# Optimization experiments

Hardware: AMD Instinct MI355X
Metric: run time of the kernel (lower is better)

Reference implementation:

```python
import jax, jax.numpy as jnp
import numpy as np

B, N, H, Z, C, IN = 4, 32768, 512, 256, 9, 64
N_TRUNK = 4   # fc_2..fc_5
N_HEADS = 4   # xyz, rgb, scale, opacity (n_layers=1 each)
FACTORS = {'xyz': 1.0, 'rgb': 1.0, 'scale': 1.0, 'opacity': 1.0}


def setup_inputs() -> dict:
    key = jax.random.key(0)
    ks = jax.random.split(key, 20)
    rn = lambda k, s, sc=1.0: jax.random.normal(k, s, jnp.float32) * np.float32(sc)
    wg = 1.0 / np.sqrt(H)       # ModLinear weight_gain / sqrt(in_features)
    sg = 1.0 / np.sqrt(Z)       # style-linear init scale
    inp = {
        'pt_feat': rn(ks[0], (B, N, IN)),
        'onehots': jax.random.uniform(ks[1], (B, N, C), jnp.float32),
        'z': rn(ks[2], (B, Z)),
        'fc1_w': rn(ks[3], (H, IN), 1.0 / np.sqrt(IN)),
        'fc1_b': jnp.zeros((H,), jnp.float32),
        'fcma_w': rn(ks[4], (H, C), 1.0 / np.sqrt(C)),
        # stacked ModLinear params: fc_2..fc_5
        'trunk_weight': rn(ks[5], (N_TRUNK, H, H), wg),
        'trunk_walpha': rn(ks[6], (N_TRUNK, H, Z), sg),
        'trunk_balpha': jnp.ones((N_TRUNK, H), jnp.float32),
        'trunk_wbeta': rn(ks[7], (N_TRUNK, H, Z), sg),
        'trunk_bbeta': jnp.zeros((N_TRUNK, H), jnp.float32),
        # stacked ModLinear params: fc_6_{xyz,rgb,scale,opacity}_0
        'head_weight': rn(ks[8], (N_HEADS, H, H), wg),
        'head_walpha': rn(ks[9], (N_HEADS, H, Z), sg),
        'head_balpha': jnp.ones((N_HEADS, H), jnp.float32),
        'head_wbeta': rn(ks[10], (N_HEADS, H, Z), sg),
        'head_bbeta': jnp.zeros((N_HEADS, H), jnp.float32),
        # output heads
        'out_w_xyz': rn(ks[11], (3, H), 1.0 / np.sqrt(H)),
        'out_b_xyz': jnp.zeros((3,), jnp.float32),
        'out_w_rgb': rn(ks[12], (3, H), 1.0 / np.sqrt(H)),
        'out_b_rgb': jnp.zeros((3,), jnp.float32),
        'out_w_scale': rn(ks[13], (3, H), 1.0 / np.sqrt(H)),
        'out_b_scale': jnp.zeros((3,), jnp.float32),
        'out_w_opacity': rn(ks[14], (1, H), 1.0 / np.sqrt(H)),
        'out_b_opacity': jnp.zeros((1,), jnp.float32),
    }
    return inp


def _act(x):
    # LeakyReLU(0.2)
    return jnp.where(x > 0, x, 0.2 * x)


def _modlin(x, z, W, Wa, ba, Wb, bb):
    """ModLinear with bias=False, mod_bias=True, output_mode=True.
    torch: baddbmm(beta, x, (W*alpha).T) == (x*alpha) @ W.T + beta
    x: [B,N,H], z: [B,Z], W: [H,H], Wa/Wb: [H,Z], ba/bb: [H]."""
    alpha = z @ Wa.T + ba            # [B,H] per-batch input scale
    beta = z @ Wb.T + bb             # [B,H] per-batch output bias
    y = jnp.einsum('bni,oi->bno', x * alpha[:, None, :], W)
    return y + beta[:, None, :]


def reference(pt_feat, onehots, z, fc1_w, fc1_b, fcma_w,
              trunk_weight, trunk_walpha, trunk_balpha, trunk_wbeta, trunk_bbeta,
              head_weight, head_walpha, head_balpha, head_wbeta, head_bbeta,
              out_w_xyz, out_b_xyz, out_w_rgb, out_b_rgb,
              out_w_scale, out_b_scale, out_w_opacity, out_b_opacity):
    f = _act(pt_feat @ fc1_w.T + fc1_b + onehots @ fcma_w.T)  # [B,N,H]
    for i in range(N_TRUNK):
        f = _act(_modlin(f, z, trunk_weight[i], trunk_walpha[i], trunk_balpha[i],
                         trunk_wbeta[i], trunk_bbeta[i]))
    heads = [(out_w_xyz, out_b_xyz), (out_w_rgb, out_b_rgb),
             (out_w_scale, out_b_scale), (out_w_opacity, out_b_opacity)]
    outs = []
    for i, (ow, ob) in enumerate(heads):
        g = _act(_modlin(f, z, head_weight[i], head_walpha[i], head_balpha[i],
                         head_wbeta[i], head_bbeta[i]))
        outs.append(g @ ow.T + ob)
    xyz = (jax.nn.sigmoid(outs[0]) - 0.5) * FACTORS['xyz']
    rgb = outs[1] * FACTORS['rgb']
    scale = jnp.clip(outs[2], 1.0, 1.0)
    opacity = jax.nn.sigmoid(outs[3]) * FACTORS['opacity'] + (1.0 - FACTORS['opacity'])
    # concat dict values in fixed key order (xyz,rgb,scale,opacity) -> [B,N,10]
    return jnp.concatenate([xyz, rgb, scale, opacity], axis=-1)
```

## Files before the change

### kernel.cpp

```cpp
#include <hip/hip_runtime.h>
#include <hip/hip_bf16.h>
#include <cstdint>

#define MTOT 131072
#define MC2  65536
#define MCH  32768
#define HDIM 512

typedef _Float16 f16x8 __attribute__((ext_vector_type(8)));
typedef _Float16 f16x4 __attribute__((ext_vector_type(4)));
typedef unsigned short u16x8 __attribute__((ext_vector_type(8)));
typedef unsigned short u16x4 __attribute__((ext_vector_type(4)));
typedef float    f32x4 __attribute__((ext_vector_type(4)));

__device__ __forceinline__ float bf2f(unsigned short u) {
  return __uint_as_float(((unsigned)u) << 16);
}

__device__ __forceinline__ float ldin(const void* p, long i, int isbf) {
  if (isbf) return bf2f(((const unsigned short*)p)[i]);
  return ((const float*)p)[i];
}

__device__ __forceinline__ void load_lds16(const void* g, void* lds) {
  __builtin_amdgcn_global_load_lds(
      (const __attribute__((address_space(1))) void*)(unsigned long long)(uintptr_t)g,
      (__attribute__((address_space(3))) void*)(unsigned int)(uintptr_t)lds,
      16, 0, 0);
}

__global__ void detect_k(const unsigned* __restrict__ balpha, int* __restrict__ flag) {
  if (threadIdx.x == 0) flag[0] = (balpha[0] == 0x3F803F80u) ? 1 : 0;
}

__global__ __launch_bounds__(256)
void prep_ab(const void* __restrict__ z,
             const void* __restrict__ twa, const void* __restrict__ tba,
             const void* __restrict__ twb, const void* __restrict__ tbb,
             const void* __restrict__ hwa, const void* __restrict__ hba,
             const void* __restrict__ hwb, const void* __restrict__ hbb,
             const int* __restrict__ flag,
             float* __restrict__ alphas, float* __restrict__ betas) {
  const int isbf = flag[0];
  const int bid = blockIdx.x;
  const int og = bid & 7, rest = bid >> 3;
  const int l = rest >> 3, p = (rest >> 2) & 1, b = rest & 3;
  __shared__ float zs[256];
  zs[threadIdx.x] = ldin(z, b * 256 + threadIdx.x, isbf);
  __syncthreads();
  const void *Wsrc, *bsrc;
  long wofs, bofs;
  if (l < 4) {
    Wsrc = (p ? twb : twa); wofs = (long)l * 512 * 256;
    bsrc = (p ? tbb : tba); bofs = l * 512;
  } else {
    const int h = (l == 6) ? 3 : (l - 4);
    Wsrc = (p ? hwb : hwa); wofs = (long)h * 512 * 256;
    bsrc = (p ? hbb : hba); bofs = h * 512;
  }
  const int o = og * 64 + (threadIdx.x >> 2);
  const int kq = threadIdx.x & 3;
  float s = 0.f;
  if (isbf) {
    const unsigned short* wp = (const unsigned short*)Wsrc + wofs + (long)o * 256 + kq * 64;
#pragma unroll
    for (int g = 0; g < 8; g++) {
      u16x8 v = *(const u16x8*)(wp + g * 8);
#pragma unroll
      for (int j = 0; j < 8; j++) s += zs[kq * 64 + g * 8 + j] * bf2f(v[j]);
    }
  } else {
    const float* wp = (const float*)Wsrc + wofs + (long)o * 256 + kq * 64;
#pragma unroll
    for (int g = 0; g < 16; g++) {
      f32x4 v = *(const f32x4*)(wp + g * 4);
#pragma unroll
      for (int j = 0; j < 4; j++) s += zs[kq * 64 + g * 4 + j] * v[j];
    }
  }
  s += __shfl_xor(s, 1, 64);
  s += __shfl_xor(s, 2, 64);
  if (kq == 0) {
    float* dst = (p ? betas : alphas) + (l * 4 + b) * 512;
    dst[o] = s + ldin(bsrc, bofs + o, isbf);
  }
}

__global__ void wmod_k(const void* __restrict__ tw, const void* __restrict__ hw,
                       const int* __restrict__ flag,
                       const float* __restrict__ alphas, _Float16* __restrict__ wmod) {
  const int isbf = flag[0];
  const long t = (long)blockIdx.x * 256 + threadIdx.x;
  const long idx = t * 8;
  const int l   = (int)(idx >> 20);
  const long r0 = idx & ((1 << 20) - 1);
  const int b   = (int)(r0 >> 18);
  const int o   = (int)((r0 >> 9) & 511);
  const int k0  = (int)(r0 & 511);
  const void* wsrc; long ofs;
  if (l < 4) { wsrc = tw; ofs = ((long)l << 18) + (o << 9) + k0; }
  else { const int h = (l == 6) ? 3 : (l - 4); wsrc = hw; ofs = ((long)h << 18) + (o << 9) + k0; }
  const float* al = alphas + (l * 4 + b) * 512 + k0;
  f32x4 a0 = *(const f32x4*)(al);
  f32x4 a1 = *(const f32x4*)(al + 4);
  f16x8 d;
  if (isbf) {
    u16x8 w8 = *(const u16x8*)((const unsigned short*)wsrc + ofs);
#pragma unroll
    for (int j = 0; j < 4; j++) d[j] = (_Float16)(bf2f(w8[j]) * a0[j]);
#pragma unroll
    for (int j = 0; j < 4; j++) d[4 + j] = (_Float16)(bf2f(w8[4 + j]) * a1[j]);
  } else {
    f32x4 w0 = *(const f32x4*)((const float*)wsrc + ofs);
    f32x4 w1 = *(const f32x4*)((const float*)wsrc + ofs + 4);
#pragma unroll
    for (int j = 0; j < 4; j++) d[j] = (_Float16)(w0[j] * a0[j]);
#pragma unroll
    for (int j = 0; j < 4; j++) d[4 + j] = (_Float16)(w1[j] * a1[j]);
  }
  *(f16x8*)(wmod + ((long)(l * 4 + b) << 18) + (o << 9) + k0) = d;
}

__global__ __launch_bounds__(256)
void pack_x(const void* __restrict__ pt, const void* __restrict__ oh,
            long pt_ofs, long oh_ofs, const int* __restrict__ flag,
            _Float16* __restrict__ X) {
  const int isbf = flag[0];
  const int m = blockIdx.x * 8 + (threadIdx.x >> 5);
  const int c5 = threadIdx.x & 31;
  f16x4 d;
  if (c5 < 16) {
    if (isbf) {
      u16x4 v = *(const u16x4*)((const unsigned short*)pt + pt_ofs + (long)m * 64 + c5 * 4);
#pragma unroll
      for (int j = 0; j < 4; j++) d[j] = (_Float16)bf2f(v[j]);
    } else {
      f32x4 v = *(const f32x4*)((const float*)pt + pt_ofs + (long)m * 64 + c5 * 4);
#pragma unroll
      for (int j = 0; j < 4; j++) d[j] = (_Float16)v[j];
    }
  } else {
#pragma unroll
    for (int j = 0; j < 4; j++) {
      const int c = c5 * 4 + j;
      d[j] = (c < 73) ? (_Float16)ldin(oh, oh_ofs + (long)m * 9 + (c - 64), isbf) : (_Float16)0.f;
    }
  }
  *(f16x4*)(X + (long)m * 128 + c5 * 4) = d;
}

__global__ void pack_wc(const void* __restrict__ fc1w, const void* __restrict__ fcmaw,
                        const void* __restrict__ fc1b, const int* __restrict__ flag,
                        _Float16* __restrict__ Wc, float* __restrict__ fb32) {
  const int isbf = flag[0];
  const int o = blockIdx.x, c = threadIdx.x;
  float v = 0.f;
  if (c < 64)      v = ldin(fc1w, o * 64 + c, isbf);
  else if (c < 73) v = ldin(fcmaw, o * 9 + c - 64, isbf);
  Wc[o * 128 + c] = (_Float16)v;
  if (c == 0) fb32[o] = ldin(fc1b, o, isbf);
}

__global__ void conv_small(const void* __restrict__ owx, const void* __restrict__ owr,
                           const void* __restrict__ owo, const void* __restrict__ obx,
                           const void* __restrict__ obr, const void* __restrict__ obo,
                           const int* __restrict__ flag, float* __restrict__ dst) {
  const int t = blockIdx.x * 256 + threadIdx.x;
  if (t >= 3591) return;
  const int isbf = flag[0];
  float v;
  if (t < 1536)      v = ldin(owx, t, isbf);
  else if (t < 3072) v = ldin(owr, t - 1536, isbf);
  else if (t < 3584) v = ldin(owo, t - 3072, isbf);
  else if (t < 3587) v = ldin(obx, t - 3584, isbf);
  else if (t < 3590) v = ldin(obr, t - 3587, isbf);
  else               v = ldin(obo, 0, isbf);
  dst[t] = v;
}

__global__ __launch_bounds__(256)
void gemm_k(const _Float16* __restrict__ A, int lda, int K,
            const _Float16* __restrict__ Wb, int ldb, long wstride,
            const float* __restrict__ biasb, int bstride,
            _Float16* __restrict__ C) {
  __shared__ __align__(16) short As[2 * 128 * 32];
  __shared__ __align__(16) short Bs[2 * 128 * 32];
  const int tid = threadIdx.x;
  const int wave = tid >> 6, lane = tid & 63;
  const int zr = blockIdx.z * MCH;
  const int m0 = blockIdx.x * 128;
  const int n0 = blockIdx.y * 128;
  const _Float16* W = Wb + (long)blockIdx.z * wstride;
  const float* bias = biasb + blockIdx.z * bstride;

  const int l4 = lane >> 2;
  const int sw4 = (lane & 3) ^ (l4 & 3);
  const _Float16* aA = A + (long)(zr + m0 + wave * 32 + l4) * lda + sw4 * 8;
  const _Float16* aB = W + (long)(n0 + wave * 32 + l4) * ldb + sw4 * 8;
  short* dA0 = &As[(wave * 32) * 32];
  short* dA1 = &As[(wave * 32 + 16) * 32];
  short* dB0 = &Bs[(wave * 32) * 32];
  short* dB1 = &Bs[(wave * 32 + 16) * 32];

  const int wm = wave >> 1, wn = wave & 1;
  const int fr = lane & 15, fq = lane >> 4;
  const int sq = (fq ^ (fr & 3)) * 8;

  f32x4 acc[4][4] = {};

  load_lds16(aA, dA0);
  load_lds16(aA + 16 * (long)lda, dA1);
  load_lds16(aB, dB0);
  load_lds16(aB + 16 * (long)ldb, dB1);

  const int nIter = K >> 5;
  for (int k = 0; k < nIter; k++) {
    const int cur = (k & 1) << 12;
    __syncthreads();
    if (k + 1 < nIter) {
      const int nxt = ((k + 1) & 1) << 12;
      const long ko = (long)(k + 1) * 32;
      load_lds16(aA + ko, dA0 + nxt);
      load_lds16(aA + ko + 16 * (long)lda, dA1 + nxt);
      load_lds16(aB + ko, dB0 + nxt);
      load_lds16(aB + ko + 16 * (long)ldb, dB1 + nxt);
    }
    f16x8 af[4], bfv[4];
#pragma unroll
    for (int i = 0; i < 4; i++)
      af[i] = *(const f16x8*)&As[cur + (wm * 64 + i * 16 + fr) * 32 + sq];
#pragma unroll
    for (int j = 0; j < 4; j++)
      bfv[j] = *(const f16x8*)&Bs[cur + (wn * 64 + j * 16 + fr) * 32 + sq];
#pragma unroll
    for (int i = 0; i < 4; i++)
#pragma unroll
      for (int j = 0; j < 4; j++)
        acc[i][j] = __builtin_amdgcn_mfma_f32_16x16x32_f16(af[i], bfv[j], acc[i][j], 0, 0, 0);
  }

#pragma unroll
  for (int j = 0; j < 4; j++) {
    const int col = n0 + wn * 64 + j * 16 + fr;
    const float bv = bias[col];
#pragma unroll
    for (int i = 0; i < 4; i++) {
      const long row = (long)zr + m0 + wm * 64 + i * 16 + fq * 4;
#pragma unroll
      for (int r = 0; r < 4; r++) {
        float v = acc[i][j][r] + bv;
        v = v > 0.f ? v : 0.2f * v;
        C[(row + r) * HDIM + col] = (_Float16)v;
      }
    }
  }
}

#define BAR() asm volatile("s_barrier" ::: "memory")
#define VMC(n) asm volatile("s_waitcnt vmcnt(" #n ")" ::: "memory")
#define PR1 __builtin_amdgcn_s_setprio(1)
#define PR0 __builtin_amdgcn_s_setprio(0)

__global__ __launch_bounds__(512, 2)
void gemm256_k(const _Float16* __restrict__ A,
               const _Float16* __restrict__ Wb, long wstride,
               const float* __restrict__ biasb, int bstride,
               _Float16* __restrict__ C) {
  __shared__ __align__(16) short As[2][16384];
  __shared__ __align__(16) short Bs[2][16384];
  const int tid = threadIdx.x;
  const int wave = tid >> 6, lane = tid & 63;
  const int gsw = (blockIdx.x & 7) * 64 + (blockIdx.x >> 3);
  const int z = gsw >> 8;
  const int n0 = (gsw & 1) * 256;
  const int m0 = ((gsw >> 1) & 127) * 256;
  const long zr = (long)z * MCH;
  const _Float16* W = Wb + (long)z * wstride;
  const float* bias = biasb + z * bstride;

  const int srow = lane >> 3;
  const int schk = (lane & 7) ^ srow;
  const _Float16* gA = A + (zr + m0 + wave * 8 + srow) * 512L + schk * 8;
  const _Float16* gB = W + ((long)(n0 + wave * 8 + srow)) * 512L + schk * 8;
  short* lA = &As[0][0] + wave * 512;
  short* lB = &Bs[0][0] + wave * 512;

#define STGA(buf, t, j) load_lds16(gA + (t) * 64 + (j) * (64 * 512L), lA + (buf) * 16384 + (j) * 4096)
#define STGB(buf, t, j) load_lds16(gB + (t) * 64 + (j) * (64 * 512L), lB + (buf) * 16384 + (j) * 4096)

  const int fr = lane & 15, fq = lane >> 4;
  const int wm = wave >> 2, wn = wave & 3;
  const int c0 = (fq ^ (fr & 7)) * 8;
  const int c1 = c0 ^ 32;
  const int aB0 = (wm * 128 + fr) * 64;
  const int bB0 = (wn * 64 + fr) * 64;

  f16x8 aF[4][2], bF[4][2];
  f32x4 acc[8][4] = {};

#define RDA(buf, i) { aF[(i) & 3][0] = *(const f16x8*)&As[buf][aB0 + (i) * 1024 + c0]; \
                      aF[(i) & 3][1] = *(const f16x8*)&As[buf][aB0 + (i) * 1024 + c1]; }
#define RDB(buf, j) { bF[j][0] = *(const f16x8*)&Bs[buf][bB0 + (j) * 1024 + c0]; \
                      bF[j][1] = *(const f16x8*)&Bs[buf][bB0 + (j) * 1024 + c1]; }
#define MMQ(ih, jh) { \
  _Pragma("unroll") for (int il = 0; il < 4; il++) \
  _Pragma("unroll") for (int jl = 0; jl < 2; jl++) { \
    acc[(ih) * 4 + il][(jh) * 2 + jl] = __builtin_amdgcn_mfma_f32_16x16x32_f16( \
        aF[il][0], bF[(jh) * 2 + jl][0], acc[(ih) * 4 + il][(jh) * 2 + jl], 0, 0, 0); \
    acc[(ih) * 4 + il][(jh) * 2 + jl] = __builtin_amdgcn_mfma_f32_16x16x32_f16( \
        aF[il][1], bF[(jh) * 2 + jl][1], acc[(ih) * 4 + il][(jh) * 2 + jl], 0, 0, 0); } }

  STGA(0, 0, 0); STGA(0, 0, 1); STGA(0, 0, 2); STGA(0, 0, 3);
  STGB(0, 0, 0); STGB(0, 0, 1); STGB(0, 0, 2); STGB(0, 0, 3);
  STGA(1, 1, 0); STGA(1, 1, 1); STGA(1, 1, 2); STGA(1, 1, 3);
  VMC(4); BAR();

#pragma unroll
  for (int t = 0; t < 8; t++) {
    const int buf = t & 1;
    RDA(buf, 0) RDA(buf, 1) RDA(buf, 2) RDA(buf, 3) RDB(buf, 0) RDB(buf, 1)
    if (t + 1 < 8) { STGB(buf ^ 1, t + 1, 0); STGB(buf ^ 1, t + 1, 1); }
    BAR(); PR1; MMQ(0, 0); PR0; BAR();
    RDB(buf, 2) RDB(buf, 3)
    if (t + 1 < 8) { STGB(buf ^ 1, t + 1, 2); STGB(buf ^ 1, t + 1, 3); }
    BAR(); PR1; MMQ(0, 1); PR0; BAR();
    RDA(buf, 4) RDA(buf, 5) RDA(buf, 6) RDA(buf, 7)
    BAR(); PR1; MMQ(1, 0); PR0; BAR();
    if (t + 2 < 8) { STGA(buf, t + 2, 0); STGA(buf, t + 2, 1); STGA(buf, t + 2, 2); STGA(buf, t + 2, 3); }
    BAR(); PR1; MMQ(1, 1); PR0;
    if (t < 6) { VMC(4); } else if (t == 6) { VMC(0); }
    BAR();
  }

#pragma unroll
  for (int j = 0; j < 4; j++) {
    const int col = n0 + wn * 64 + j * 16 + fr;
    const float bv = bias[col];
#pragma unroll
    for (int i = 0; i < 8; i++) {
      const long row = zr + m0 + wm * 128 + i * 16 + fq * 4;
#pragma unroll
      for (int r = 0; r < 4; r++) {
        float v = acc[i][j][r] + bv;
        v = v > 0.f ? v : 0.2f * v;
        C[(row + r) * HDIM + col] = (_Float16)v;
      }
    }
  }
#undef STGA
#undef STGB
#undef RDA
#undef RDB
#undef MMQ
}

template <int MODE>
__global__ __launch_bounds__(256)
void proj_k(const _Float16* __restrict__ g, const float* __restrict__ P,
            const float* __restrict__ ob, const int* __restrict__ flag,
            void* __restrict__ outv, long row0) {
  const int tid = threadIdx.x;
  const int wave = tid >> 6, lane = tid & 63;
  const int rg = lane >> 4, lg = lane & 15;
  const long row = (long)blockIdx.x * 16 + wave * 4 + rg;
  const _Float16* gr = g + row * HDIM;
  float s0 = 0.f, s1 = 0.f, s2 = 0.f;
#pragma unroll
  for (int p = 0; p < 4; p++) {
    const int c0 = p * 128 + lg * 8;
    f16x8 v = *(const f16x8*)(gr + c0);
#pragma unroll
    for (int j = 0; j < 8; j++) {
      float gv = (float)v[j];
      s0 += gv * P[c0 + j];
      if (MODE != 2) {
        s1 += gv * P[512 + c0 + j];
        s2 += gv * P[1024 + c0 + j];
      }
    }
  }
#pragma unroll
  for (int off = 1; off < 16; off <<= 1) {
    s0 += __shfl_xor(s0, off, 64);
    if (MODE != 2) {
      s1 += __shfl_xor(s1, off, 64);
      s2 += __shfl_xor(s2, off, 64);
    }
  }
  if (lg == 0) {
    const long ro = (row0 + row) * 10;
    float v[4]; int c0, nc;
    if (MODE == 0) {
      v[0] = 1.f / (1.f + __expf(-(s0 + ob[0]))) - 0.5f;
      v[1] = 1.f / (1.f + __expf(-(s1 + ob[1]))) - 0.5f;
      v[2] = 1.f / (1.f + __expf(-(s2 + ob[2]))) - 0.5f;
      c0 = 0; nc = 3;
    } else if (MODE == 1) {
      v[0] = s0 + ob[0]; v[1] = s1 + ob[1]; v[2] = s2 + ob[2];
      c0 = 3; nc = 3;
    } else {
      v[0] = 1.0f; v[1] = 1.0f; v[2] = 1.0f;
      v[3] = 1.f / (1.f + __expf(-(s0 + ob[0])));
      c0 = 6; nc = 4;
    }
    if (flag[0]) {
      __hip_bfloat16* o = (__hip_bfloat16*)outv + ro + c0;
      for (int c = 0; c < nc; c++) o[c] = __float2bfloat16(v[c]);
    } else {
      float* o = (float*)outv + ro + c0;
      for (int c = 0; c < nc; c++) o[c] = v[c];
    }
  }
}

extern "C" void kernel_launch(void* const* d_in, const int* in_sizes, int n_in,
                              void* d_out, int out_size, void* d_ws, size_t ws_size,
                              hipStream_t stream) {
  const void* pt    = d_in[0];
  const void* oh    = d_in[1];
  const void* z     = d_in[2];
  const void* fc1w  = d_in[3];
  const void* fc1b  = d_in[4];
  const void* fcmaw = d_in[5];
  const void* tw    = d_in[6];
  const void* twa   = d_in[7];
  const void* tba   = d_in[8];
  const void* twb   = d_in[9];
  const void* tbb   = d_in[10];
  const void* hw    = d_in[11];
  const void* hwa   = d_in[12];
  const void* hba   = d_in[13];
  const void* hwb   = d_in[14];
  const void* hbb   = d_in[15];
  const void* owx   = d_in[16];
  const void* obx   = d_in[17];
  const void* owr   = d_in[18];
  const void* obr   = d_in[19];
  const void* owo   = d_in[22];
  const void* obo   = d_in[23];

  char* ws = (char*)d_ws;
  _Float16* g0    = (_Float16*)(ws + 0);
  _Float16* g1    = (_Float16*)(ws + 67108864LL);
  _Float16* X     = (_Float16*)(ws + 67108864LL);
  _Float16* wmodp = (_Float16*)(ws + 134217728LL);
  _Float16* Wc    = (_Float16*)(ws + 148897792LL);
  float* alphas   = (float*)(ws + 149028864LL);
  float* betas    = (float*)(ws + 149086208LL);
  float* fb32     = (float*)(ws + 149143552LL);
  int*   dflag    = (int*)  (ws + 149145600LL);
  float* ow32     = (float*)(ws + 149145664LL);

  detect_k<<<1, 64, 0, stream>>>((const unsigned*)tba, dflag);
  prep_ab<<<448, 256, 0, stream>>>(z, twa, tba, twb, tbb, hwa, hba, hwb, hbb, dflag, alphas, betas);
  wmod_k<<<3584, 256, 0, stream>>>(tw, hw, dflag, alphas, wmodp);
  pack_wc<<<512, 128, 0, stream>>>(fc1w, fcmaw, fc1b, dflag, Wc, fb32);
  conv_small<<<15, 256, 0, stream>>>(owx, owr, owo, obx, obr, obo, dflag, ow32);

  dim3 gg(MCH / 128, 4, 2), gb(256);
  const int pgrid = MC2 / 16;
  for (int p = 0; p < 2; p++) {
    const long prow = (long)p * MC2;
    pack_x<<<MC2 / 8, 256, 0, stream>>>(pt, oh, prow * 64, prow * 9, dflag, X);
    gemm_k<<<gg, gb, 0, stream>>>(X, 128, 128, Wc, 128, 0, fb32, 0, g0);
    _Float16* fin = g0; _Float16* fout = g1;
    for (int l = 0; l < 4; l++) {
      gemm256_k<<<512, 512, 0, stream>>>(fin, wmodp + (long)(l * 4 + p * 2) * 262144, 262144,
                                         betas + (l * 4 + p * 2) * 512, 512, fout);
      _Float16* t = fin; fin = fout; fout = t;
    }
    gemm256_k<<<512, 512, 0, stream>>>(fin, wmodp + (long)(4 * 4 + p * 2) * 262144, 262144,
                                       betas + (4 * 4 + p * 2) * 512, 512, g1);
    proj_k<0><<<pgrid, 256, 0, stream>>>(g1, ow32, ow32 + 3584, dflag, d_out, prow);
    gemm256_k<<<512, 512, 0, stream>>>(fin, wmodp + (long)(5 * 4 + p * 2) * 262144, 262144,
                                       betas + (5 * 4 + p * 2) * 512, 512, g1);
    proj_k<1><<<pgrid, 256, 0, stream>>>(g1, ow32 + 1536, ow32 + 3587, dflag, d_out, prow);
    gemm256_k<<<512, 512, 0, stream>>>(fin, wmodp + (long)(6 * 4 + p * 2) * 262144, 262144,
                                       betas + (6 * 4 + p * 2) * 512, 512, g1);
    proj_k<2><<<pgrid, 256, 0, stream>>>(g1, ow32 + 3072, ow32 + 3590, dflag, d_out, prow);
  }
}
```

Measured before the change: 919.8 us.

## Split A/B fragment registers and prefetch next tile's LDS reads during MFMA

Restructures the gemm256 main loop with separate low/high register sets for A and B fragments. The next K-tile's low fragments are read from LDS while the last MFMA quadrant of the current tile runs, and the barrier count per iteration drops. The epilogue loops are reordered so each row's stores go to four columns spaced 16 apart. The extra fragment registers raise register pressure, which could hurt occupancy under launch_bounds(512,2), and the changed wait/barrier placement has to stay correct for the double-buffered LDS.

```diff
diff --git a/kernel.cpp b/kernel.cpp
--- a/kernel.cpp
+++ b/kernel.cpp
@@ -258,6 +258,8 @@
 
 #define BAR() asm volatile("s_barrier" ::: "memory")
 #define VMC(n) asm volatile("s_waitcnt vmcnt(" #n ")" ::: "memory")
+#define LGK0() do { asm volatile("s_waitcnt lgkmcnt(0)" ::: "memory"); \
+                    __builtin_amdgcn_sched_barrier(0); } while (0)
 #define PR1 __builtin_amdgcn_s_setprio(1)
 #define PR0 __builtin_amdgcn_s_setprio(0)
 
@@ -295,62 +297,80 @@
   const int aB0 = (wm * 128 + fr) * 64;
   const int bB0 = (wn * 64 + fr) * 64;
 
-  f16x8 aF[4][2], bF[4][2];
+  f16x8 aLo[4][2], aHi[4][2], bLo[2][2], bHi[2][2];
   f32x4 acc[8][4] = {};
 
-#define RDA(buf, i) { aF[(i) & 3][0] = *(const f16x8*)&As[buf][aB0 + (i) * 1024 + c0]; \
-                      aF[(i) & 3][1] = *(const f16x8*)&As[buf][aB0 + (i) * 1024 + c1]; }
-#define RDB(buf, j) { bF[j][0] = *(const f16x8*)&Bs[buf][bB0 + (j) * 1024 + c0]; \
-                      bF[j][1] = *(const f16x8*)&Bs[buf][bB0 + (j) * 1024 + c1]; }
-#define MMQ(ih, jh) { \
+#define RDAL(buf, i) { aLo[i][0] = *(const f16x8*)&As[buf][aB0 + (i) * 1024 + c0]; \
+                       aLo[i][1] = *(const f16x8*)&As[buf][aB0 + (i) * 1024 + c1]; }
+#define RDAH(buf, i) { aHi[i][0] = *(const f16x8*)&As[buf][aB0 + ((i) + 4) * 1024 + c0]; \
+                       aHi[i][1] = *(const f16x8*)&As[buf][aB0 + ((i) + 4) * 1024 + c1]; }
+#define RDBL(buf, j) { bLo[j][0] = *(const f16x8*)&Bs[buf][bB0 + (j) * 1024 + c0]; \
+                       bLo[j][1] = *(const f16x8*)&Bs[buf][bB0 + (j) * 1024 + c1]; }
+#define RDBH(buf, j) { bHi[j][0] = *(const f16x8*)&Bs[buf][bB0 + ((j) + 2) * 1024 + c0]; \
+                       bHi[j][1] = *(const f16x8*)&Bs[buf][bB0 + ((j) + 2) * 1024 + c1]; }
+#define MMQ(AF, io, BF, jo) { \
   _Pragma("unroll") for (int il = 0; il < 4; il++) \
   _Pragma("unroll") for (int jl = 0; jl < 2; jl++) { \
-    acc[(ih) * 4 + il][(jh) * 2 + jl] = __builtin_amdgcn_mfma_f32_16x16x32_f16( \
-        aF[il][0], bF[(jh) * 2 + jl][0], acc[(ih) * 4 + il][(jh) * 2 + jl], 0, 0, 0); \
-    acc[(ih) * 4 + il][(jh) * 2 + jl] = __builtin_amdgcn_mfma_f32_16x16x32_f16( \
-        aF[il][1], bF[(jh) * 2 + jl][1], acc[(ih) * 4 + il][(jh) * 2 + jl], 0, 0, 0); } }
+    acc[(io) + il][(jo) + jl] = __builtin_amdgcn_mfma_f32_16x16x32_f16( \
+        AF[il][0], BF[jl][0], acc[(io) + il][(jo) + jl], 0, 0, 0); \
+    acc[(io) + il][(jo) + jl] = __builtin_amdgcn_mfma_f32_16x16x32_f16( \
+        AF[il][1], BF[jl][1], acc[(io) + il][(jo) + jl], 0, 0, 0); } }
 
   STGA(0, 0, 0); STGA(0, 0, 1); STGA(0, 0, 2); STGA(0, 0, 3);
   STGB(0, 0, 0); STGB(0, 0, 1); STGB(0, 0, 2); STGB(0, 0, 3);
   STGA(1, 1, 0); STGA(1, 1, 1); STGA(1, 1, 2); STGA(1, 1, 3);
   VMC(4); BAR();
+  RDAL(0, 0) RDAL(0, 1) RDAL(0, 2) RDAL(0, 3) RDBL(0, 0) RDBL(0, 1)
 
 #pragma unroll
   for (int t = 0; t < 8; t++) {
     const int buf = t & 1;
-    RDA(buf, 0) RDA(buf, 1) RDA(buf, 2) RDA(buf, 3) RDB(buf, 0) RDB(buf, 1)
-    if (t + 1 < 8) { STGB(buf ^ 1, t + 1, 0); STGB(buf ^ 1, t + 1, 1); }
-    BAR(); PR1; MMQ(0, 0); PR0; BAR();
-    RDB(buf, 2) RDB(buf, 3)
-    if (t + 1 < 8) { STGB(buf ^ 1, t + 1, 2); STGB(buf ^ 1, t + 1, 3); }
-    BAR(); PR1; MMQ(0, 1); PR0; BAR();
-    RDA(buf, 4) RDA(buf, 5) RDA(buf, 6) RDA(buf, 7)
-    BAR(); PR1; MMQ(1, 0); PR0; BAR();
-    if (t + 2 < 8) { STGA(buf, t + 2, 0); STGA(buf, t + 2, 1); STGA(buf, t + 2, 2); STGA(buf, t + 2, 3); }
-    BAR(); PR1; MMQ(1, 1); PR0;
-    if (t < 6) { VMC(4); } else if (t == 6) { VMC(0); }
+    RDBH(buf, 0) RDBH(buf, 1)
+    if (t + 1 < 8) { STGB(buf ^ 1, t + 1, 0); STGB(buf ^ 1, t + 1, 1);
+                     STGB(buf ^ 1, t + 1, 2); STGB(buf ^ 1, t + 1, 3); }
+    PR1; MMQ(aLo, 0, bLo, 0); PR0;
     BAR();
-  }
-
-#pragma unroll
-  for (int j = 0; j < 4; j++) {
-    const int col = n0 + wn * 64 + j * 16 + fr;
-    const float bv = bias[col];
-#pragma unroll
-    for (int i = 0; i < 8; i++) {
-      const long row = zr + m0 + wm * 128 + i * 16 + fq * 4;
-#pragma unroll
-      for (int r = 0; r < 4; r++) {
-        float v = acc[i][j][r] + bv;
+    RDAH(buf, 0) RDAH(buf, 1) RDAH(buf, 2) RDAH(buf, 3)
+    PR1; MMQ(aLo, 0, bHi, 2); PR0;
+    VMC(4);
+    BAR();
+    PR1; MMQ(aHi, 4, bLo, 0); PR0;
+    VMC(0);
+    LGK0();
+    BAR();
+    if (t + 2 < 8) { STGA(buf, t + 2, 0); STGA(buf, t + 2, 1);
+                     STGA(buf, t + 2, 2); STGA(buf, t + 2, 3); }
+    if (t + 1 < 8) {
+      RDAL(buf ^ 1, 0) RDAL(buf ^ 1, 1) RDAL(buf ^ 1, 2) RDAL(buf ^ 1, 3)
+      RDBL(buf ^ 1, 0) RDBL(buf ^ 1, 1)
+    }
+    PR1; MMQ(aHi, 4, bHi, 2); PR0;
+    BAR();
+  }
+
+  float bv[4];
+#pragma unroll
+  for (int j = 0; j < 4; j++) bv[j] = bias[n0 + wn * 64 + j * 16 + fr];
+#pragma unroll
+  for (int i = 0; i < 8; i++) {
+    const long row = zr + m0 + wm * 128 + i * 16 + fq * 4;
+#pragma unroll
+    for (int r = 0; r < 4; r++) {
+      _Float16* cp = C + (row + r) * HDIM + n0 + wn * 64 + fr;
+#pragma unroll
+      for (int j = 0; j < 4; j++) {
+        float v = acc[i][j][r] + bv[j];
         v = v > 0.f ? v : 0.2f * v;
-        C[(row + r) * HDIM + col] = (_Float16)v;
+        cp[j * 16] = (_Float16)v;
       }
     }
   }
 #undef STGA
 #undef STGB
-#undef RDA
-#undef RDB
+#undef RDAL
+#undef RDAH
+#undef RDBL
+#undef RDBH
 #undef MMQ
 }
 
```

After: 887.1 us. 1.04x faster.
